# Kernel optimization log

Measured on AMD Instinct MI355X. Metric: run time of the kernel, lower is better.

The kernel has to match this reference:

```python
import jax, jax.numpy as jnp
from jax import lax
import numpy as np

B, T, D_IN, H, OUT = 64, 512, 512, 1024, 128


def setup_inputs() -> dict:
    key = jax.random.key(0)
    ks = jax.random.split(key, 12)
    s = 0.02
    return {
        "x": jax.random.normal(ks[0], (B, T, D_IN), dtype=jnp.float32),
        "W_ih0": jax.random.normal(ks[1], (H, D_IN), dtype=jnp.float32) * s,
        "W_hh0": jax.random.normal(ks[2], (H, H), dtype=jnp.float32) * s,
        "b_ih0": jax.random.normal(ks[3], (H,), dtype=jnp.float32) * s,
        "b_hh0": jax.random.normal(ks[4], (H,), dtype=jnp.float32) * s,
        "W_ih1": jax.random.normal(ks[5], (H, H), dtype=jnp.float32) * s,
        "W_hh1": jax.random.normal(ks[6], (H, H), dtype=jnp.float32) * s,
        "b_ih1": jax.random.normal(ks[7], (H,), dtype=jnp.float32) * s,
        "b_hh1": jax.random.normal(ks[8], (H,), dtype=jnp.float32) * s,
        "W_fc": jax.random.normal(ks[9], (OUT, H), dtype=jnp.float32) * s,
        "b_fc": jax.random.normal(ks[10], (OUT,), dtype=jnp.float32) * s,
    }


def _rnn_layer(seq, W_ih, W_hh, b_ih, b_hh):
    # seq: [B, T, D] -> outputs [B, T, H]; h_t = tanh(x_t W_ih^T + b_ih + h_{t-1} W_hh^T + b_hh)
    pre = jnp.einsum("btd,hd->bth", seq, W_ih) + b_ih + b_hh  # one big input GEMM
    h0 = jnp.zeros((seq.shape[0], W_hh.shape[0]), dtype=seq.dtype)

    def step(h, p_t):
        h_new = jnp.tanh(p_t + h @ W_hh.T)
        return h_new, h_new

    _, hs = lax.scan(step, h0, jnp.swapaxes(pre, 0, 1))  # [T, B, H]
    return jnp.swapaxes(hs, 0, 1)  # [B, T, H]


def reference(x, W_ih0, W_hh0, b_ih0, b_hh0, W_ih1, W_hh1, b_ih1, b_hh1, W_fc, b_fc):
    h1 = _rnn_layer(x, W_ih0, W_hh0, b_ih0, b_hh0)
    h2 = _rnn_layer(h1, W_ih1, W_hh1, b_ih1, b_hh1)
    last = h2[:, -1, :]  # [B, H]
    return last @ W_fc.T + b_fc  # [B, OUT]
```

## Files before the change

kernel.cpp:

```cpp
#include <hip/hip_runtime.h>
#include <stdint.h>
#include <stddef.h>

#define Bn   64
#define Tn   512
#define DINn 512
#define Hn   1024
#define OUTn 128

typedef __attribute__((ext_vector_type(4))) float f32x4;
typedef __attribute__((ext_vector_type(8))) short short8;
typedef __attribute__((ext_vector_type(4))) unsigned int u32x4;

__device__ __forceinline__ unsigned short f2bf(float f){
  unsigned int x = __builtin_bit_cast(unsigned int, f);
  x += 0x7fffu + ((x >> 16) & 1u);
  return (unsigned short)(x >> 16);
}
__device__ __forceinline__ float bf2f(unsigned short u){
  return __builtin_bit_cast(float, (unsigned int)u << 16);
}
__device__ __forceinline__ float tanh_fast(float v){
  float e = __expf(2.0f * v);
  return 1.0f - 2.0f / (e + 1.0f);
}

template<bool FAST>
__device__ __forceinline__ void st16(unsigned short* p, u32x4 v){
  if constexpr (FAST)
    asm volatile("global_store_dwordx4 %0, %1, off sc0" :: "v"(p), "v"(v) : "memory");
  else
    asm volatile("global_store_dwordx4 %0, %1, off sc0 sc1" :: "v"(p), "v"(v) : "memory");
}
__device__ __forceinline__ unsigned atom_poll(unsigned int* p){
  unsigned old, zero = 0;
  asm volatile("global_atomic_add %0, %1, %2, off sc0\n\t"
               "s_waitcnt vmcnt(0)"
               : "=&v"(old) : "v"(p), "v"(zero) : "memory");
  return old;
}
__device__ __forceinline__ void atom_poll2(unsigned int* p1, unsigned int* p2,
                                           unsigned &v1, unsigned &v2){
  unsigned zero = 0;
  asm volatile("global_atomic_add %0, %2, %4, off sc0\n\t"
               "global_atomic_add %1, %3, %4, off sc0\n\t"
               "s_waitcnt vmcnt(0)"
               : "=&v"(v1), "=&v"(v2)
               : "v"(p1), "v"(p2), "v"(zero) : "memory");
}
__device__ __forceinline__ void atom_inc(unsigned int* p){
  unsigned one = 1;
  asm volatile("global_atomic_add %0, %1, off" :: "v"(p), "v"(one) : "memory");
}
__device__ __forceinline__ unsigned ld1_sc0(const unsigned int* p){
  unsigned v;
  asm volatile("global_load_dword %0, %1, off sc0\n\t"
               "s_waitcnt vmcnt(0)" : "=&v"(v) : "v"(p) : "memory");
  return v;
}
__device__ __forceinline__ unsigned umin4(u32x4 a){
  unsigned m0 = a[0] < a[1] ? a[0] : a[1];
  unsigned m1 = a[2] < a[3] ? a[2] : a[3];
  return m0 < m1 ? m0 : m1;
}
__device__ __forceinline__ unsigned ld_line8_slow(const unsigned int* p){
  u32x4 a, b;
  asm volatile("global_load_dwordx4 %0, %2, off sc0 sc1\n\t"
               "global_load_dwordx4 %1, %3, off sc0 sc1\n\t"
               "s_waitcnt vmcnt(0)"
               : "=&v"(a), "=&v"(b) : "v"(p), "v"(p + 4) : "memory");
  unsigned ma = umin4(a), mb = umin4(b);
  return ma < mb ? ma : mb;
}
template<bool FAST>
__device__ __forceinline__ void wait_one(unsigned int* fc, unsigned int* fl, unsigned wf8, unsigned wslow){
  if constexpr (FAST){
    if (!wf8) return;
    for (int i = 0; i < (1 << 16); ++i){
      if (atom_poll(fc) >= wf8) return;
      __builtin_amdgcn_s_sleep(2);
    }
  } else {
    if (!wslow) return;
    for (int i = 0; i < (1 << 16); ++i){
      if (ld_line8_slow(fl) >= wslow) return;
      if (i > 16) __builtin_amdgcn_s_sleep(1);
    }
  }
}
template<bool FAST>
__device__ __forceinline__ void wait_dual(unsigned int* fc1, unsigned int* fl1, unsigned wf1, unsigned ws1,
                                          unsigned int* fc2, unsigned int* fl2, unsigned wf2, unsigned ws2){
  if constexpr (FAST){
    if (!wf2){ wait_one<true>(fc1, fl1, wf1, ws1); return; }
    for (int i = 0; i < (1 << 16); ++i){
      unsigned v1, v2;
      atom_poll2(fc1, fc2, v1, v2);
      if (v1 >= wf1 && v2 >= wf2) return;
      __builtin_amdgcn_s_sleep(2);
    }
  } else {
    if (!ws2){ wait_one<false>(fc1, fl1, wf1, ws1); return; }
    for (int i = 0; i < (1 << 16); ++i){
      if (ld_line8_slow(fl1) >= ws1 && ld_line8_slow(fl2) >= ws2) return;
      if (i > 16) __builtin_amdgcn_s_sleep(1);
    }
  }
}

template<bool FAST>
__device__ __forceinline__ void stage_lin(const unsigned short* base, unsigned short* hl, int tid){
  const unsigned short* p0 = base + (size_t)tid * 8;
  const unsigned short* p1 = p0 + 512 * 8;
  u32x4 v0, v1;
  if constexpr (FAST)
    asm volatile("global_load_dwordx4 %0, %2, off sc0\n\t"
                 "global_load_dwordx4 %1, %3, off sc0\n\t"
                 "s_waitcnt vmcnt(0)"
                 : "=&v"(v0), "=&v"(v1) : "v"(p0), "v"(p1) : "memory");
  else
    asm volatile("global_load_dwordx4 %0, %2, off sc0 sc1\n\t"
                 "global_load_dwordx4 %1, %3, off sc0 sc1\n\t"
                 "s_waitcnt vmcnt(0)"
                 : "=&v"(v0), "=&v"(v1) : "v"(p0), "v"(p1) : "memory");
  *(u32x4*)((char*)hl + tid * 16) = v0;
  *(u32x4*)((char*)hl + tid * 16 + 8192) = v1;
}
template<bool FAST>
__device__ __forceinline__ void ld4_chunk(const unsigned short* p, float* pv){
  unsigned u0,u1,u2,u3;
  if constexpr (FAST)
    asm volatile("global_load_ushort %0, %4, off sc0\n\t"
                 "global_load_ushort %1, %5, off sc0\n\t"
                 "global_load_ushort %2, %6, off sc0\n\t"
                 "global_load_ushort %3, %7, off sc0\n\t"
                 "s_waitcnt vmcnt(0)"
                 : "=&v"(u0), "=&v"(u1), "=&v"(u2), "=&v"(u3)
                 : "v"(p), "v"(p + 8), "v"(p + 16), "v"(p + 24) : "memory");
  else
    asm volatile("global_load_ushort %0, %4, off sc0 sc1\n\t"
                 "global_load_ushort %1, %5, off sc0 sc1\n\t"
                 "global_load_ushort %2, %6, off sc0 sc1\n\t"
                 "global_load_ushort %3, %7, off sc0 sc1\n\t"
                 "s_waitcnt vmcnt(0)"
                 : "=&v"(u0), "=&v"(u1), "=&v"(u2), "=&v"(u3)
                 : "v"(p), "v"(p + 8), "v"(p + 16), "v"(p + 24) : "memory");
  pv[0] = bf2f((unsigned short)u0); pv[1] = bf2f((unsigned short)u1);
  pv[2] = bf2f((unsigned short)u2); pv[3] = bf2f((unsigned short)u3);
}

__device__ __forceinline__ f32x4 mfma_tile(const char* lbase, const short8* wf, int lrow, int kh){
  f32x4 a0 = {0.f,0.f,0.f,0.f}, a1 = a0, a2 = a0, a3 = a0;
  int rb = kh * 128 + lrow * 16;
#pragma unroll
  for (int kk = 0; kk < 8; ++kk)
    a0 = __builtin_amdgcn_mfma_f32_16x16x32_bf16(*(const short8*)(lbase + kk*512 + rb), wf[kk], a0, 0,0,0);
#pragma unroll
  for (int kk = 8; kk < 16; ++kk)
    a1 = __builtin_amdgcn_mfma_f32_16x16x32_bf16(*(const short8*)(lbase + kk*512 + rb), wf[kk], a1, 0,0,0);
#pragma unroll
  for (int kk = 16; kk < 24; ++kk)
    a2 = __builtin_amdgcn_mfma_f32_16x16x32_bf16(*(const short8*)(lbase + kk*512 + rb), wf[kk], a2, 0,0,0);
#pragma unroll
  for (int kk = 24; kk < 32; ++kk)
    a3 = __builtin_amdgcn_mfma_f32_16x16x32_bf16(*(const short8*)(lbase + kk*512 + rb), wf[kk], a3, 0,0,0);
  return (a0 + a1) + (a2 + a3);
}

__global__ void cvt_bf16x8(const float* __restrict__ in, unsigned short* __restrict__ out,
                           long long n8){
  long long i = (long long)blockIdx.x * blockDim.x + threadIdx.x;
  long long stride = (long long)gridDim.x * blockDim.x;
  for (; i < n8; i += stride){
    const float* p = in + i*8;
    float4 a = *(const float4*)p;
    float4 b = *(const float4*)(p+4);
    short8 v;
    v[0]=(short)f2bf(a.x); v[1]=(short)f2bf(a.y); v[2]=(short)f2bf(a.z); v[3]=(short)f2bf(a.w);
    v[4]=(short)f2bf(b.x); v[5]=(short)f2bf(b.y); v[6]=(short)f2bf(b.z); v[7]=(short)f2bf(b.w);
    *(short8*)(out + i*8) = v;
  }
}

__global__ void bias_combine(const float* __restrict__ a, const float* __restrict__ b, float* __restrict__ o,
                             const float* __restrict__ c, const float* __restrict__ d, float* __restrict__ p){
  int i = blockIdx.x * blockDim.x + threadIdx.x;
  if (i < Hn){ o[i] = a[i] + b[i]; p[i] = c[i] + d[i]; }
}

__launch_bounds__(256, 2)
__global__ void gemm_pre0(const float* __restrict__ Av, const unsigned short* __restrict__ Bm,
                          const float* __restrict__ bias, unsigned short* __restrict__ C,
                          int N, int K)
{
  __shared__ unsigned short lA[128*64];
  __shared__ unsigned short lB[128*64];
  int bn = blockIdx.x, bm = blockIdx.y;
  int m0 = bm*128, n0 = bn*128;
  int tid = threadIdx.x, lane = tid & 63, w = tid >> 6;
  int wm = (w >> 1)*64, wn = (w & 1)*64;
  int cl = lane & 15, kh = lane >> 4;

  f32x4 acc[4][4];
  f32x4 z = {0.f,0.f,0.f,0.f};
#pragma unroll
  for (int i=0;i<4;i++)
#pragma unroll
    for (int j=0;j<4;j++) acc[i][j]=z;

  for (int k0 = 0; k0 < K; k0 += 64){
    __syncthreads();
#pragma unroll
    for (int r = 0; r < 4; ++r){
      int c = r*256 + tid;
      int row = c >> 3, cof = (c & 7)*8;
      const float* ap = Av + (size_t)(m0+row)*K + k0 + cof;
      float4 a = *(const float4*)ap;
      float4 b = *(const float4*)(ap+4);
      short8 v;
      v[0]=(short)f2bf(a.x); v[1]=(short)f2bf(a.y); v[2]=(short)f2bf(a.z); v[3]=(short)f2bf(a.w);
      v[4]=(short)f2bf(b.x); v[5]=(short)f2bf(b.y); v[6]=(short)f2bf(b.z); v[7]=(short)f2bf(b.w);
      *(short8*)&lA[row*64 + cof] = v;
      const unsigned short* bp = Bm + (size_t)(n0+row)*K + k0 + cof;
      *(short8*)&lB[row*64 + cof] = *(const short8*)bp;
    }
    __syncthreads();
#pragma unroll
    for (int kk = 0; kk < 2; ++kk){
      int kb = kk*32 + kh*8;
      short8 af[4], bfr[4];
#pragma unroll
      for (int i=0;i<4;i++) af[i]  = *(const short8*)&lA[(wm + i*16 + cl)*64 + kb];
#pragma unroll
      for (int j=0;j<4;j++) bfr[j] = *(const short8*)&lB[(wn + j*16 + cl)*64 + kb];
#pragma unroll
      for (int i=0;i<4;i++)
#pragma unroll
        for (int j=0;j<4;j++)
          acc[i][j] = __builtin_amdgcn_mfma_f32_16x16x32_bf16(af[i], bfr[j], acc[i][j], 0,0,0);
    }
  }
#pragma unroll
  for (int j=0;j<4;j++){
    int n = n0 + wn + j*16 + cl;
    float bs = bias[n];
#pragma unroll
    for (int i=0;i<4;i++){
      int mr = m0 + wm + i*16 + kh*4;
#pragma unroll
      for (int e=0;e<4;e++){
        int m = mr + e;
        int b = m >> 9, t = m & (Tn-1);
        C[((size_t)t*Bn + b)*N + n] = f2bf(acc[i][j][e] + bs);
      }
    }
  }
}

template<bool FAST>
__device__ __forceinline__ void rnn_body(
    int role, int g, int slot, int tid, int w, int lane, int cl, int kh, int lrow,
    const unsigned short* pre0, unsigned short* bufP, unsigned short* h1buf,
    const float* bias1,
    unsigned int* FCA0, unsigned int* FCA1, unsigned int* FCB, unsigned int* FCC,
    unsigned int* FLA, unsigned int* FLB, unsigned int* FLC,
    const short8* wf, unsigned short* hl, unsigned short* outl)
{
  const char* lbase = (const char*)hl;
  int n0 = slot*128 + w*16;
  int olocal = w*128 + ((cl>>3)*8 + kh*4)*8 + (cl&7);
  unsigned int* myFL = ((role == 0) ? FLA : (role == 1) ? FLB : FLC) + slot;

  for (int t = 0; t < Tn; ++t){
    float pv[4] = {0.f,0.f,0.f,0.f};
    if (role == 0 && kh < 2){
      const unsigned short* pp = pre0 + ((size_t)t*Bn + g*8 + kh*4)*Hn + n0 + cl;
#pragma unroll
      for (int j=0;j<4;j++) pv[j] = bf2f(pp[(size_t)j*Hn]);
    }
    if (tid == 0){
      if (role == 0)      wait_one <FAST>(FCA0, FLA, 8u*(unsigned)t, (unsigned)t);
      else if (role == 1) wait_one <FAST>(FCA1, FLA, 8u*(unsigned)(t+1), (unsigned)(t+1));
      else                wait_dual<FAST>(FCB, FLB, 8u*(unsigned)(t+1), (unsigned)(t+1),
                                          FCC, FLC, 8u*(unsigned)t, (unsigned)t);
    }
    __syncthreads();
    bool staged = true;
    if (role == 0){
      if (t > 0) stage_lin<FAST>(h1buf + ((size_t)(t+1)*8 + g)*8192, hl, tid);
      else staged = false;
    } else if (role == 1){
      stage_lin<FAST>(h1buf + ((size_t)(t+2)*8 + g)*8192, hl, tid);
    } else {
      if (kh < 2)
        ld4_chunk<FAST>(h1buf + ((size_t)t*8 + g)*8192 + slot*1024 + ((w*16+cl)>>3)*64 + kh*32 + (cl&7), pv);
      if (t > 0) stage_lin<FAST>(bufP + ((size_t)(t-1)*Bn + g*8)*Hn, hl, tid);
      else staged = false;
    }
    __syncthreads();
    f32x4 acc = {0.f,0.f,0.f,0.f};
    if (staged) acc = mfma_tile(lbase, wf, lrow, kh);
    if (kh < 2){
      float bs = (role == 1) ? bias1[n0 + cl] : 0.f;
#pragma unroll
      for (int j=0;j<4;j++){
        float v = acc[j] + pv[j] + bs;
        if (role != 1) v = tanh_fast(v);
        outl[olocal + j*8] = f2bf(v);
      }
    }
    unsigned short* tile;
    if (role == 0)      tile = h1buf + ((size_t)(t+2)*8 + g)*8192;
    else if (role == 1) tile = h1buf + ((size_t)t*8 + g)*8192;
    else                tile = bufP + ((size_t)t*Bn + g*8)*Hn;
    if (lane < 16){
      u32x4 v = *(const u32x4*)(outl + w*128 + lane*8);
      st16<FAST>(tile + slot*1024 + (w*16 + lane)*8, v);
    }
    asm volatile("s_waitcnt vmcnt(0)" ::: "memory");
    __syncthreads();
    if (tid == 0){
      if constexpr (FAST){
        if (role == 0){ atom_inc(FCA0); atom_inc(FCA1); }
        else if (role == 1) atom_inc(FCB);
        else atom_inc(FCC);
      } else {
        asm volatile("global_store_dword %0, %1, off sc0 sc1" :: "v"(myFL), "v"((unsigned)(t+1)) : "memory");
      }
    }
  }
}

__launch_bounds__(512, 2)
__global__ void rnn_fused(const unsigned short* __restrict__ pre0_ro,
                          unsigned short* __restrict__ bufP,
                          unsigned short* __restrict__ h1buf,
                          const float* __restrict__ Whh0,
                          const float* __restrict__ Wih1,
                          const float* __restrict__ Whh1,
                          const float* __restrict__ bias1,
                          unsigned int* ctrs)
{
  __shared__ __align__(16) unsigned short hl[8192];
  __shared__ __align__(16) unsigned short outl[1024];
  __shared__ int s_fast;
  int bx = blockIdx.x;
  int g = bx & 7;
  int sub = bx >> 3;
  int role = sub >> 3, slot = sub & 7;
  int tid = threadIdx.x, lane = tid & 63, w = tid >> 6;
  int n0 = slot*128 + w*16;
  int cl = lane & 15, kh = lane >> 4, lrow = cl & 7;
  unsigned int* FLA = ctrs + (0*8 + g)*32;
  unsigned int* FLB = ctrs + (1*8 + g)*32;
  unsigned int* FLC = ctrs + (2*8 + g)*32;
  unsigned int* arrive1 = ctrs + 768;
  unsigned int* badf    = ctrs + 772;
  unsigned int* arrive2 = ctrs + 776;
  unsigned int* FCA0 = ctrs + 1536 + (0*8 + g)*32;
  unsigned int* FCB  = ctrs + 1536 + (1*8 + g)*32;
  unsigned int* FCC  = ctrs + 1536 + (2*8 + g)*32;
  unsigned int* FCA1 = ctrs + 1536 + (3*8 + g)*32;

  if (tid == 0){
    int xcc;
    asm volatile("s_getreg_b32 %0, hwreg(HW_REG_XCC_ID)" : "=s"(xcc));
    unsigned int* testw = ctrs + 1024 + g*32;
    unsigned int* armed = testw + 16;
    if (xcc != g)
      __hip_atomic_fetch_or(badf, 1u, __ATOMIC_RELAXED, __HIP_MEMORY_SCOPE_AGENT);
    __hip_atomic_fetch_add(arrive1, 1u, __ATOMIC_ACQ_REL, __HIP_MEMORY_SCOPE_AGENT);
    int t1 = 0;
    for (int i = 0; i < (1 << 20); ++i){
      if (__hip_atomic_load(arrive1, __ATOMIC_ACQUIRE, __HIP_MEMORY_SCOPE_AGENT) >= 192u){ t1 = 1; break; }
      __builtin_amdgcn_s_sleep(2);
    }
    if (!t1) __hip_atomic_fetch_or(badf, 1u, __ATOMIC_RELAXED, __HIP_MEMORY_SCOPE_AGENT);
    unsigned magic = 0xC0FFEE00u | (unsigned)g;
    if (sub == 0){
      asm volatile("global_store_dword %0, %1, off sc0\n\t"
                   "s_waitcnt vmcnt(0)" :: "v"(testw), "v"(magic) : "memory");
      atom_inc(armed);
    }
    int ok = 0;
    for (int i = 0; i < (1 << 15); ++i){
      if (atom_poll(armed) >= 1u){ ok = (ld1_sc0(testw) == magic); break; }
      if (i > 16) __builtin_amdgcn_s_sleep(1);
    }
    if (!ok) __hip_atomic_fetch_or(badf, 1u, __ATOMIC_RELAXED, __HIP_MEMORY_SCOPE_AGENT);
    __hip_atomic_fetch_add(arrive2, 1u, __ATOMIC_ACQ_REL, __HIP_MEMORY_SCOPE_AGENT);
    int t2 = 0;
    for (int i = 0; i < (1 << 20); ++i){
      if (__hip_atomic_load(arrive2, __ATOMIC_ACQUIRE, __HIP_MEMORY_SCOPE_AGENT) >= 192u){ t2 = 1; break; }
      __builtin_amdgcn_s_sleep(2);
    }
    unsigned bad = __hip_atomic_load(badf, __ATOMIC_ACQUIRE, __HIP_MEMORY_SCOPE_AGENT);
    s_fast = (t2 && bad == 0u) ? 1 : 0;
  }
  __syncthreads();
  const bool fast = (s_fast != 0);

  const float* Wmat = (role == 0) ? Whh0 : (role == 1) ? Wih1 : Whh1;
  short8 wf[32];
  {
    const float* wr = Wmat + (size_t)(n0 + cl)*Hn + kh*8;
#pragma unroll
    for (int kk = 0; kk < 32; ++kk){
      float4 a = *(const float4*)(wr + kk*32);
      float4 b = *(const float4*)(wr + kk*32 + 4);
      short8 v;
      v[0]=(short)f2bf(a.x); v[1]=(short)f2bf(a.y); v[2]=(short)f2bf(a.z); v[3]=(short)f2bf(a.w);
      v[4]=(short)f2bf(b.x); v[5]=(short)f2bf(b.y); v[6]=(short)f2bf(b.z); v[7]=(short)f2bf(b.w);
      wf[kk] = v;
    }
  }

  if (fast)
    rnn_body<true >(role, g, slot, tid, w, lane, cl, kh, lrow, pre0_ro, bufP, h1buf,
                    bias1, FCA0, FCA1, FCB, FCC, FLA, FLB, FLC, wf, hl, outl);
  else
    rnn_body<false>(role, g, slot, tid, w, lane, cl, kh, lrow, pre0_ro, bufP, h1buf,
                    bias1, FCA0, FCA1, FCB, FCC, FLA, FLB, FLC, wf, hl, outl);
}

__global__ void fc_k(const unsigned short* __restrict__ bufP,
                     const float* __restrict__ Wfc, const float* __restrict__ bfc,
                     float* __restrict__ out)
{
  int gw = (blockIdx.x * blockDim.x + threadIdx.x) >> 6;
  int lane = threadIdx.x & 63;
  int b = gw >> 7, o = gw & 127;
  const unsigned short* tile = bufP + ((size_t)(Tn-1)*Bn + (b & ~7))*Hn;
  int r = b & 7;
  const float* wr = Wfc + (size_t)o*Hn;
  float s = 0.f;
  for (int k = lane; k < Hn; k += 64)
    s += bf2f(tile[((k>>3)*8 + r)*8 + (k&7)]) * wr[k];
#pragma unroll
  for (int off = 32; off > 0; off >>= 1) s += __shfl_down(s, off, 64);
  if (lane == 0) out[b*OUTn + o] = s + bfc[o];
}

extern "C" void kernel_launch(void* const* d_in, const int* in_sizes, int n_in,
                              void* d_out, int out_size, void* d_ws, size_t ws_size,
                              hipStream_t stream)
{
  const float* x    = (const float*)d_in[0];
  const float* Wih0 = (const float*)d_in[1];
  const float* Whh0 = (const float*)d_in[2];
  const float* bih0 = (const float*)d_in[3];
  const float* bhh0 = (const float*)d_in[4];
  const float* Wih1 = (const float*)d_in[5];
  const float* Whh1 = (const float*)d_in[6];
  const float* bih1 = (const float*)d_in[7];
  const float* bhh1 = (const float*)d_in[8];
  const float* Wfc  = (const float*)d_in[9];
  const float* bfc  = (const float*)d_in[10];
  float* out = (float*)d_out;

  unsigned short* bufP  = (unsigned short*)d_ws;
  unsigned short* h1buf = bufP  + (size_t)Bn*Tn*Hn;
  unsigned short* wih0b = h1buf + (size_t)(Tn+2)*8*8192;
  float* bias0 = (float*)(wih0b + (size_t)Hn*DINn);
  float* bias1 = bias0 + Hn;
  unsigned int* ctrs = (unsigned int*)(bias1 + Hn);

  hipMemsetAsync(ctrs, 0, 4096*sizeof(unsigned int), stream);

  cvt_bf16x8<<<256, 256, 0, stream>>>(Wih0, wih0b, (long long)Hn*DINn/8);
  bias_combine<<<4, 256, 0, stream>>>(bih0, bhh0, bias0, bih1, bhh1, bias1);

  dim3 g1(Hn/128, (Bn*Tn)/128);
  gemm_pre0<<<g1, 256, 0, stream>>>(x, wih0b, bias0, bufP, Hn, DINn);

  rnn_fused<<<192, 512, 0, stream>>>(bufP, bufP, h1buf, Whh0, Wih1, Whh1, bias1, ctrs);

  fc_k<<<2048, 256, 0, stream>>>(bufP, Wfc, bfc, out);
}
```

Measured before the change: 1.384 ms.

## Merge layer-1 input projection into layer-0 blocks and drop the third role

The layer-1 input-GEMM role is folded into the layer-0 workgroups. Each layer-0 block now holds both W_hh0 and W_ih1 fragments in registers and computes the projection of the previous h1 right after publishing the current h1 step. This cuts the grid from 192 to 128 blocks and removes one handoff hop. It also switches to per-wave arrival counters (64 per step), which drops the block-wide barrier before signaling. Layer-1 now fetches its h1 projection and staged tile in a single combined load batch, and the spin-wait sleeps less aggressively. The cost is doubled register pressure from the second weight set (launch bounds drop to 1 block per SM) and more serial work per layer-0 step on the critical recurrence path.

```diff
diff --git a/kernel.cpp b/kernel.cpp
--- a/kernel.cpp
+++ b/kernel.cpp
@@ -73,12 +73,12 @@
   return ma < mb ? ma : mb;
 }
 template<bool FAST>
-__device__ __forceinline__ void wait_one(unsigned int* fc, unsigned int* fl, unsigned wf8, unsigned wslow){
+__device__ __forceinline__ void wait_one(unsigned int* fc, unsigned int* fl, unsigned wfast, unsigned wslow){
   if constexpr (FAST){
-    if (!wf8) return;
+    if (!wfast) return;
     for (int i = 0; i < (1 << 16); ++i){
-      if (atom_poll(fc) >= wf8) return;
-      __builtin_amdgcn_s_sleep(2);
+      if (atom_poll(fc) >= wfast) return;
+      if (i > 8) __builtin_amdgcn_s_sleep(1);
     }
   } else {
     if (!wslow) return;
@@ -97,7 +97,7 @@
       unsigned v1, v2;
       atom_poll2(fc1, fc2, v1, v2);
       if (v1 >= wf1 && v2 >= wf2) return;
-      __builtin_amdgcn_s_sleep(2);
+      if (i > 8) __builtin_amdgcn_s_sleep(1);
     }
   } else {
     if (!ws2){ wait_one<false>(fc1, fl1, wf1, ws1); return; }
@@ -111,7 +111,7 @@
 template<bool FAST>
 __device__ __forceinline__ void stage_lin(const unsigned short* base, unsigned short* hl, int tid){
   const unsigned short* p0 = base + (size_t)tid * 8;
-  const unsigned short* p1 = p0 + 512 * 8;
+  const unsigned short* p1 = p0 + 4096;
   u32x4 v0, v1;
   if constexpr (FAST)
     asm volatile("global_load_dwordx4 %0, %2, off sc0\n\t"
@@ -125,6 +125,39 @@
                  : "=&v"(v0), "=&v"(v1) : "v"(p0), "v"(p1) : "memory");
   *(u32x4*)((char*)hl + tid * 16) = v0;
   *(u32x4*)((char*)hl + tid * 16 + 8192) = v1;
+}
+template<bool FAST>
+__device__ __forceinline__ void stage_ld4(const unsigned short* base, unsigned short* hl, int tid,
+                                          const unsigned short* p4, float* pv){
+  const unsigned short* p0 = base + (size_t)tid * 8;
+  const unsigned short* p1 = p0 + 4096;
+  u32x4 v0, v1; unsigned u0,u1,u2,u3;
+  if constexpr (FAST)
+    asm volatile(
+      "global_load_dwordx4 %0, %6, off sc0\n\t"
+      "global_load_dwordx4 %1, %7, off sc0\n\t"
+      "global_load_ushort %2, %8, off sc0\n\t"
+      "global_load_ushort %3, %9, off sc0\n\t"
+      "global_load_ushort %4, %10, off sc0\n\t"
+      "global_load_ushort %5, %11, off sc0\n\t"
+      "s_waitcnt vmcnt(0)"
+      : "=&v"(v0),"=&v"(v1),"=&v"(u0),"=&v"(u1),"=&v"(u2),"=&v"(u3)
+      : "v"(p0),"v"(p1),"v"(p4),"v"(p4+8),"v"(p4+16),"v"(p4+24) : "memory");
+  else
+    asm volatile(
+      "global_load_dwordx4 %0, %6, off sc0 sc1\n\t"
+      "global_load_dwordx4 %1, %7, off sc0 sc1\n\t"
+      "global_load_ushort %2, %8, off sc0 sc1\n\t"
+      "global_load_ushort %3, %9, off sc0 sc1\n\t"
+      "global_load_ushort %4, %10, off sc0 sc1\n\t"
+      "global_load_ushort %5, %11, off sc0 sc1\n\t"
+      "s_waitcnt vmcnt(0)"
+      : "=&v"(v0),"=&v"(v1),"=&v"(u0),"=&v"(u1),"=&v"(u2),"=&v"(u3)
+      : "v"(p0),"v"(p1),"v"(p4),"v"(p4+8),"v"(p4+16),"v"(p4+24) : "memory");
+  *(u32x4*)((char*)hl + tid * 16) = v0;
+  *(u32x4*)((char*)hl + tid * 16 + 8192) = v1;
+  pv[0] = bf2f((unsigned short)u0); pv[1] = bf2f((unsigned short)u1);
+  pv[2] = bf2f((unsigned short)u2); pv[3] = bf2f((unsigned short)u3);
 }
 template<bool FAST>
 __device__ __forceinline__ void ld4_chunk(const unsigned short* p, float* pv){
@@ -262,76 +295,119 @@
     int role, int g, int slot, int tid, int w, int lane, int cl, int kh, int lrow,
     const unsigned short* pre0, unsigned short* bufP, unsigned short* h1buf,
     const float* bias1,
-    unsigned int* FCA0, unsigned int* FCA1, unsigned int* FCB, unsigned int* FCC,
+    unsigned int* FCA, unsigned int* FCB, unsigned int* FCC,
     unsigned int* FLA, unsigned int* FLB, unsigned int* FLC,
-    const short8* wf, unsigned short* hl, unsigned short* outl)
+    const short8* wf, const short8* wf2, unsigned short* hl, unsigned short* outl)
 {
   const char* lbase = (const char*)hl;
   int n0 = slot*128 + w*16;
   int olocal = w*128 + ((cl>>3)*8 + kh*4)*8 + (cl&7);
-  unsigned int* myFL = ((role == 0) ? FLA : (role == 1) ? FLB : FLC) + slot;
-
-  for (int t = 0; t < Tn; ++t){
-    float pv[4] = {0.f,0.f,0.f,0.f};
-    if (role == 0 && kh < 2){
-      const unsigned short* pp = pre0 + ((size_t)t*Bn + g*8 + kh*4)*Hn + n0 + cl;
-#pragma unroll
-      for (int j=0;j<4;j++) pv[j] = bf2f(pp[(size_t)j*Hn]);
-    }
-    if (tid == 0){
-      if (role == 0)      wait_one <FAST>(FCA0, FLA, 8u*(unsigned)t, (unsigned)t);
-      else if (role == 1) wait_one <FAST>(FCA1, FLA, 8u*(unsigned)(t+1), (unsigned)(t+1));
-      else                wait_dual<FAST>(FCB, FLB, 8u*(unsigned)(t+1), (unsigned)(t+1),
-                                          FCC, FLC, 8u*(unsigned)t, (unsigned)t);
-    }
+  int khc = kh & 1;
+  int p4off = slot*1024 + ((w*16+cl)>>3)*64 + khc*32 + (cl&7);
+
+  if (role == 0){
+    float bs1 = bias1[n0 + cl];
+    for (int t = 0; t < Tn; ++t){
+      float pv[4] = {0.f,0.f,0.f,0.f};
+      if (kh < 2){
+        const unsigned short* pp = pre0 + ((size_t)t*Bn + g*8 + kh*4)*Hn + n0 + cl;
+#pragma unroll
+        for (int j=0;j<4;j++) pv[j] = bf2f(pp[(size_t)j*Hn]);
+      }
+      if (tid == 0) wait_one<FAST>(FCA, FLA, 64u*(unsigned)t, (unsigned)t);
+      __syncthreads();
+      if (t > 0) stage_lin<FAST>(h1buf + ((size_t)(t+1)*8 + g)*8192, hl, tid);
+      __syncthreads();
+      f32x4 acc = {0.f,0.f,0.f,0.f};
+      if (t > 0) acc = mfma_tile(lbase, wf, lrow, kh);
+      if (kh < 2){
+#pragma unroll
+        for (int j=0;j<4;j++) outl[olocal + j*8] = f2bf(tanh_fast(acc[j] + pv[j]));
+      }
+      unsigned short* tile = h1buf + ((size_t)(t+2)*8 + g)*8192;
+      if (lane < 16)
+        st16<FAST>(tile + slot*1024 + (w*16 + lane)*8, *(const u32x4*)(outl + w*128 + lane*8));
+      asm volatile("s_waitcnt vmcnt(0)" ::: "memory");
+      if constexpr (FAST){
+        if (lane == 0) atom_inc(FCA);
+      } else {
+        __syncthreads();
+        if (tid == 0)
+          asm volatile("global_store_dword %0, %1, off sc0 sc1" :: "v"(FLA+slot), "v"((unsigned)(t+1)) : "memory");
+      }
+      if (t > 0){
+        f32x4 acc2 = mfma_tile(lbase, wf2, lrow, kh);
+        if (kh < 2){
+#pragma unroll
+          for (int j=0;j<4;j++) outl[olocal + j*8] = f2bf(acc2[j] + bs1);
+        }
+        unsigned short* ptile = h1buf + ((size_t)(t-1)*8 + g)*8192;
+        if (lane < 16)
+          st16<FAST>(ptile + slot*1024 + (w*16 + lane)*8, *(const u32x4*)(outl + w*128 + lane*8));
+        asm volatile("s_waitcnt vmcnt(0)" ::: "memory");
+        if constexpr (FAST){
+          if (lane == 0) atom_inc(FCB);
+        } else {
+          __syncthreads();
+          if (tid == 0)
+            asm volatile("global_store_dword %0, %1, off sc0 sc1" :: "v"(FLB+slot), "v"((unsigned)t) : "memory");
+        }
+      }
+    }
+    if (tid == 0) wait_one<FAST>(FCA, FLA, 64u*(unsigned)Tn, (unsigned)Tn);
     __syncthreads();
-    bool staged = true;
-    if (role == 0){
-      if (t > 0) stage_lin<FAST>(h1buf + ((size_t)(t+1)*8 + g)*8192, hl, tid);
-      else staged = false;
-    } else if (role == 1){
-      stage_lin<FAST>(h1buf + ((size_t)(t+2)*8 + g)*8192, hl, tid);
+    stage_lin<FAST>(h1buf + ((size_t)(Tn+1)*8 + g)*8192, hl, tid);
+    __syncthreads();
+    f32x4 acc2 = mfma_tile(lbase, wf2, lrow, kh);
+    if (kh < 2){
+#pragma unroll
+      for (int j=0;j<4;j++) outl[olocal + j*8] = f2bf(acc2[j] + bs1);
+    }
+    unsigned short* ptile = h1buf + ((size_t)(Tn-1)*8 + g)*8192;
+    if (lane < 16)
+      st16<FAST>(ptile + slot*1024 + (w*16 + lane)*8, *(const u32x4*)(outl + w*128 + lane*8));
+    asm volatile("s_waitcnt vmcnt(0)" ::: "memory");
+    if constexpr (FAST){
+      if (lane == 0) atom_inc(FCB);
     } else {
-      if (kh < 2)
-        ld4_chunk<FAST>(h1buf + ((size_t)t*8 + g)*8192 + slot*1024 + ((w*16+cl)>>3)*64 + kh*32 + (cl&7), pv);
-      if (t > 0) stage_lin<FAST>(bufP + ((size_t)(t-1)*Bn + g*8)*Hn, hl, tid);
-      else staged = false;
-    }
-    __syncthreads();
-    f32x4 acc = {0.f,0.f,0.f,0.f};
-    if (staged) acc = mfma_tile(lbase, wf, lrow, kh);
-    if (kh < 2){
-      float bs = (role == 1) ? bias1[n0 + cl] : 0.f;
-#pragma unroll
-      for (int j=0;j<4;j++){
-        float v = acc[j] + pv[j] + bs;
-        if (role != 1) v = tanh_fast(v);
-        outl[olocal + j*8] = f2bf(v);
-      }
-    }
-    unsigned short* tile;
-    if (role == 0)      tile = h1buf + ((size_t)(t+2)*8 + g)*8192;
-    else if (role == 1) tile = h1buf + ((size_t)t*8 + g)*8192;
-    else                tile = bufP + ((size_t)t*Bn + g*8)*Hn;
-    if (lane < 16){
-      u32x4 v = *(const u32x4*)(outl + w*128 + lane*8);
-      st16<FAST>(tile + slot*1024 + (w*16 + lane)*8, v);
-    }
-    asm volatile("s_waitcnt vmcnt(0)" ::: "memory");
-    __syncthreads();
-    if (tid == 0){
+      __syncthreads();
+      if (tid == 0)
+        asm volatile("global_store_dword %0, %1, off sc0 sc1" :: "v"(FLB+slot), "v"((unsigned)Tn) : "memory");
+    }
+  } else {
+    for (int t = 0; t < Tn; ++t){
+      if (tid == 0) wait_dual<FAST>(FCB, FLB, 64u*(unsigned)(t+1), (unsigned)(t+1),
+                                    FCC, FLC, 64u*(unsigned)t, (unsigned)t);
+      __syncthreads();
+      float pv[4] = {0.f,0.f,0.f,0.f};
+      const unsigned short* p4 = h1buf + ((size_t)t*8 + g)*8192 + p4off;
+      if (t > 0)
+        stage_ld4<FAST>(bufP + ((size_t)(t-1)*Bn + g*8)*Hn, hl, tid, p4, pv);
+      else
+        ld4_chunk<FAST>(p4, pv);
+      __syncthreads();
+      f32x4 acc = {0.f,0.f,0.f,0.f};
+      if (t > 0) acc = mfma_tile(lbase, wf, lrow, kh);
+      if (kh < 2){
+#pragma unroll
+        for (int j=0;j<4;j++) outl[olocal + j*8] = f2bf(tanh_fast(acc[j] + pv[j]));
+      }
+      unsigned short* tile = bufP + ((size_t)t*Bn + g*8)*Hn;
+      if (lane < 16)
+        st16<FAST>(tile + slot*1024 + (w*16 + lane)*8, *(const u32x4*)(outl + w*128 + lane*8));
+      asm volatile("s_waitcnt vmcnt(0)" ::: "memory");
       if constexpr (FAST){
-        if (role == 0){ atom_inc(FCA0); atom_inc(FCA1); }
-        else if (role == 1) atom_inc(FCB);
-        else atom_inc(FCC);
+        if (lane == 0) atom_inc(FCC);
       } else {
-        asm volatile("global_store_dword %0, %1, off sc0 sc1" :: "v"(myFL), "v"((unsigned)(t+1)) : "memory");
-      }
-    }
-  }
-}
-
-__launch_bounds__(512, 2)
+        __syncthreads();
+        if (tid == 0)
+          asm volatile("global_store_dword %0, %1, off sc0 sc1" :: "v"(FLC+slot), "v"((unsigned)(t+1)) : "memory");
+      }
+    }
+  }
+}
+
+__launch_bounds__(512, 1)
 __global__ void rnn_fused(const unsigned short* __restrict__ pre0_ro,
                           unsigned short* __restrict__ bufP,
                           unsigned short* __restrict__ h1buf,
@@ -357,10 +433,9 @@
   unsigned int* arrive1 = ctrs + 768;
   unsigned int* badf    = ctrs + 772;
   unsigned int* arrive2 = ctrs + 776;
-  unsigned int* FCA0 = ctrs + 1536 + (0*8 + g)*32;
-  unsigned int* FCB  = ctrs + 1536 + (1*8 + g)*32;
-  unsigned int* FCC  = ctrs + 1536 + (2*8 + g)*32;
-  unsigned int* FCA1 = ctrs + 1536 + (3*8 + g)*32;
+  unsigned int* FCA = ctrs + 1536 + (0*8 + g)*32;
+  unsigned int* FCB = ctrs + 1536 + (1*8 + g)*32;
+  unsigned int* FCC = ctrs + 1536 + (2*8 + g)*32;
 
   if (tid == 0){
     int xcc;
@@ -372,7 +447,7 @@
     __hip_atomic_fetch_add(arrive1, 1u, __ATOMIC_ACQ_REL, __HIP_MEMORY_SCOPE_AGENT);
     int t1 = 0;
     for (int i = 0; i < (1 << 20); ++i){
-      if (__hip_atomic_load(arrive1, __ATOMIC_ACQUIRE, __HIP_MEMORY_SCOPE_AGENT) >= 192u){ t1 = 1; break; }
+      if (__hip_atomic_load(arrive1, __ATOMIC_ACQUIRE, __HIP_MEMORY_SCOPE_AGENT) >= 128u){ t1 = 1; break; }
       __builtin_amdgcn_s_sleep(2);
     }
     if (!t1) __hip_atomic_fetch_or(badf, 1u, __ATOMIC_RELAXED, __HIP_MEMORY_SCOPE_AGENT);
@@ -391,7 +466,7 @@
     __hip_atomic_fetch_add(arrive2, 1u, __ATOMIC_ACQ_REL, __HIP_MEMORY_SCOPE_AGENT);
     int t2 = 0;
     for (int i = 0; i < (1 << 20); ++i){
-      if (__hip_atomic_load(arrive2, __ATOMIC_ACQUIRE, __HIP_MEMORY_SCOPE_AGENT) >= 192u){ t2 = 1; break; }
+      if (__hip_atomic_load(arrive2, __ATOMIC_ACQUIRE, __HIP_MEMORY_SCOPE_AGENT) >= 128u){ t2 = 1; break; }
       __builtin_amdgcn_s_sleep(2);
     }
     unsigned bad = __hip_atomic_load(badf, __ATOMIC_ACQUIRE, __HIP_MEMORY_SCOPE_AGENT);
@@ -400,8 +475,8 @@
   __syncthreads();
   const bool fast = (s_fast != 0);
 
-  const float* Wmat = (role == 0) ? Whh0 : (role == 1) ? Wih1 : Whh1;
-  short8 wf[32];
+  const float* Wmat = (role == 0) ? Whh0 : Whh1;
+  short8 wf[32], wf2[32];
   {
     const float* wr = Wmat + (size_t)(n0 + cl)*Hn + kh*8;
 #pragma unroll
@@ -414,13 +489,25 @@
       wf[kk] = v;
     }
   }
+  if (role == 0){
+    const float* wr = Wih1 + (size_t)(n0 + cl)*Hn + kh*8;
+#pragma unroll
+    for (int kk = 0; kk < 32; ++kk){
+      float4 a = *(const float4*)(wr + kk*32);
+      float4 b = *(const float4*)(wr + kk*32 + 4);
+      short8 v;
+      v[0]=(short)f2bf(a.x); v[1]=(short)f2bf(a.y); v[2]=(short)f2bf(a.z); v[3]=(short)f2bf(a.w);
+      v[4]=(short)f2bf(b.x); v[5]=(short)f2bf(b.y); v[6]=(short)f2bf(b.z); v[7]=(short)f2bf(b.w);
+      wf2[kk] = v;
+    }
+  }
 
   if (fast)
     rnn_body<true >(role, g, slot, tid, w, lane, cl, kh, lrow, pre0_ro, bufP, h1buf,
-                    bias1, FCA0, FCA1, FCB, FCC, FLA, FLB, FLC, wf, hl, outl);
+                    bias1, FCA, FCB, FCC, FLA, FLB, FLC, wf, wf2, hl, outl);
   else
     rnn_body<false>(role, g, slot, tid, w, lane, cl, kh, lrow, pre0_ro, bufP, h1buf,
-                    bias1, FCA0, FCA1, FCB, FCC, FLA, FLB, FLC, wf, hl, outl);
+                    bias1, FCA, FCB, FCC, FLA, FLB, FLC, wf, wf2, hl, outl);
 }
 
 __global__ void fc_k(const unsigned short* __restrict__ bufP,
@@ -473,7 +560,7 @@
   dim3 g1(Hn/128, (Bn*Tn)/128);
   gemm_pre0<<<g1, 256, 0, stream>>>(x, wih0b, bias0, bufP, Hn, DINn);
 
-  rnn_fused<<<192, 512, 0, stream>>>(bufP, bufP, h1buf, Whh0, Wih1, Whh1, bias1, ctrs);
+  rnn_fused<<<128, 512, 0, stream>>>(bufP, bufP, h1buf, Whh0, Wih1, Whh1, bias1, ctrs);
 
   fc_k<<<2048, 256, 0, stream>>>(bufP, Wfc, bfc, out);
 }
```

After: 3.580 ms. +158.7%, slower.

## Split K across waves with LDS reduction and read h tiles directly from global

Applied to the files above, without the earlier changes.

Restructures the persistent RNN step so each wave computes two 16-column output tiles over half of K. MFMA A-operands are read straight from the global h buffer instead of being staged into LDS. A small LDS reduction then combines the two K halves, and only the first four waves apply bias and tanh and store. The change removes the LDS staging copy and one barrier-bound global-to-LDS pass per step. The trade is a partial-sum reduction, non-coherent-qualified direct global loads for the operands, and polling that spins with shorter sleeps.

```diff
diff --git a/kernel.cpp b/kernel.cpp
--- a/kernel.cpp
+++ b/kernel.cpp
@@ -23,6 +23,13 @@
 __device__ __forceinline__ float tanh_fast(float v){
   float e = __expf(2.0f * v);
   return 1.0f - 2.0f / (e + 1.0f);
+}
+__device__ __forceinline__ short8 packw(const float* p){
+  float4 a = *(const float4*)p; float4 b = *(const float4*)(p + 4);
+  short8 v;
+  v[0]=(short)f2bf(a.x); v[1]=(short)f2bf(a.y); v[2]=(short)f2bf(a.z); v[3]=(short)f2bf(a.w);
+  v[4]=(short)f2bf(b.x); v[5]=(short)f2bf(b.y); v[6]=(short)f2bf(b.z); v[7]=(short)f2bf(b.w);
+  return v;
 }
 
 template<bool FAST>
@@ -73,12 +80,12 @@
   return ma < mb ? ma : mb;
 }
 template<bool FAST>
-__device__ __forceinline__ void wait_one(unsigned int* fc, unsigned int* fl, unsigned wf8, unsigned wslow){
+__device__ __forceinline__ void wait_one(unsigned int* fc, unsigned int* fl, unsigned wfast, unsigned wslow){
   if constexpr (FAST){
-    if (!wf8) return;
+    if (!wfast) return;
     for (int i = 0; i < (1 << 16); ++i){
-      if (atom_poll(fc) >= wf8) return;
-      __builtin_amdgcn_s_sleep(2);
+      if (atom_poll(fc) >= wfast) return;
+      if (i > 8) __builtin_amdgcn_s_sleep(1);
     }
   } else {
     if (!wslow) return;
@@ -97,7 +104,7 @@
       unsigned v1, v2;
       atom_poll2(fc1, fc2, v1, v2);
       if (v1 >= wf1 && v2 >= wf2) return;
-      __builtin_amdgcn_s_sleep(2);
+      if (i > 8) __builtin_amdgcn_s_sleep(1);
     }
   } else {
     if (!ws2){ wait_one<false>(fc1, fl1, wf1, ws1); return; }
@@ -106,65 +113,6 @@
       if (i > 16) __builtin_amdgcn_s_sleep(1);
     }
   }
-}
-
-template<bool FAST>
-__device__ __forceinline__ void stage_lin(const unsigned short* base, unsigned short* hl, int tid){
-  const unsigned short* p0 = base + (size_t)tid * 8;
-  const unsigned short* p1 = p0 + 512 * 8;
-  u32x4 v0, v1;
-  if constexpr (FAST)
-    asm volatile("global_load_dwordx4 %0, %2, off sc0\n\t"
-                 "global_load_dwordx4 %1, %3, off sc0\n\t"
-                 "s_waitcnt vmcnt(0)"
-                 : "=&v"(v0), "=&v"(v1) : "v"(p0), "v"(p1) : "memory");
-  else
-    asm volatile("global_load_dwordx4 %0, %2, off sc0 sc1\n\t"
-                 "global_load_dwordx4 %1, %3, off sc0 sc1\n\t"
-                 "s_waitcnt vmcnt(0)"
-                 : "=&v"(v0), "=&v"(v1) : "v"(p0), "v"(p1) : "memory");
-  *(u32x4*)((char*)hl + tid * 16) = v0;
-  *(u32x4*)((char*)hl + tid * 16 + 8192) = v1;
-}
-template<bool FAST>
-__device__ __forceinline__ void ld4_chunk(const unsigned short* p, float* pv){
-  unsigned u0,u1,u2,u3;
-  if constexpr (FAST)
-    asm volatile("global_load_ushort %0, %4, off sc0\n\t"
-                 "global_load_ushort %1, %5, off sc0\n\t"
-                 "global_load_ushort %2, %6, off sc0\n\t"
-                 "global_load_ushort %3, %7, off sc0\n\t"
-                 "s_waitcnt vmcnt(0)"
-                 : "=&v"(u0), "=&v"(u1), "=&v"(u2), "=&v"(u3)
-                 : "v"(p), "v"(p + 8), "v"(p + 16), "v"(p + 24) : "memory");
-  else
-    asm volatile("global_load_ushort %0, %4, off sc0 sc1\n\t"
-                 "global_load_ushort %1, %5, off sc0 sc1\n\t"
-                 "global_load_ushort %2, %6, off sc0 sc1\n\t"
-                 "global_load_ushort %3, %7, off sc0 sc1\n\t"
-                 "s_waitcnt vmcnt(0)"
-                 : "=&v"(u0), "=&v"(u1), "=&v"(u2), "=&v"(u3)
-                 : "v"(p), "v"(p + 8), "v"(p + 16), "v"(p + 24) : "memory");
-  pv[0] = bf2f((unsigned short)u0); pv[1] = bf2f((unsigned short)u1);
-  pv[2] = bf2f((unsigned short)u2); pv[3] = bf2f((unsigned short)u3);
-}
-
-__device__ __forceinline__ f32x4 mfma_tile(const char* lbase, const short8* wf, int lrow, int kh){
-  f32x4 a0 = {0.f,0.f,0.f,0.f}, a1 = a0, a2 = a0, a3 = a0;
-  int rb = kh * 128 + lrow * 16;
-#pragma unroll
-  for (int kk = 0; kk < 8; ++kk)
-    a0 = __builtin_amdgcn_mfma_f32_16x16x32_bf16(*(const short8*)(lbase + kk*512 + rb), wf[kk], a0, 0,0,0);
-#pragma unroll
-  for (int kk = 8; kk < 16; ++kk)
-    a1 = __builtin_amdgcn_mfma_f32_16x16x32_bf16(*(const short8*)(lbase + kk*512 + rb), wf[kk], a1, 0,0,0);
-#pragma unroll
-  for (int kk = 16; kk < 24; ++kk)
-    a2 = __builtin_amdgcn_mfma_f32_16x16x32_bf16(*(const short8*)(lbase + kk*512 + rb), wf[kk], a2, 0,0,0);
-#pragma unroll
-  for (int kk = 24; kk < 32; ++kk)
-    a3 = __builtin_amdgcn_mfma_f32_16x16x32_bf16(*(const short8*)(lbase + kk*512 + rb), wf[kk], a3, 0,0,0);
-  return (a0 + a1) + (a2 + a3);
 }
 
 __global__ void cvt_bf16x8(const float* __restrict__ in, unsigned short* __restrict__ out,
@@ -264,19 +212,25 @@
     const float* bias1,
     unsigned int* FCA0, unsigned int* FCA1, unsigned int* FCB, unsigned int* FCC,
     unsigned int* FLA, unsigned int* FLB, unsigned int* FLC,
-    const short8* wf, unsigned short* hl, unsigned short* outl)
+    const short8* wfA, const short8* wfB,
+    unsigned short* outl, f32x4 (*red)[32])
 {
-  const char* lbase = (const char*)hl;
-  int n0 = slot*128 + w*16;
-  int olocal = w*128 + ((cl>>3)*8 + kh*4)*8 + (cl&7);
+  int t0 = 2*(w & 3);
+  int kb = (w >> 2) * 16;
+  int oA = t0*128 + ((cl>>3)*8 + kh*4)*8 + (cl&7);
   unsigned int* myFL = ((role == 0) ? FLA : (role == 1) ? FLB : FLC) + slot;
+  float bsA = 0.f, bsB = 0.f;
+  if (role == 1){
+    bsA = bias1[slot*128 + t0*16 + cl];
+    bsB = bias1[slot*128 + t0*16 + 16 + cl];
+  }
 
   for (int t = 0; t < Tn; ++t){
-    float pv[4] = {0.f,0.f,0.f,0.f};
-    if (role == 0 && kh < 2){
-      const unsigned short* pp = pre0 + ((size_t)t*Bn + g*8 + kh*4)*Hn + n0 + cl;
-#pragma unroll
-      for (int j=0;j<4;j++) pv[j] = bf2f(pp[(size_t)j*Hn]);
+    float pvA[4] = {0.f,0.f,0.f,0.f}, pvB[4] = {0.f,0.f,0.f,0.f};
+    if (role == 0 && w < 4 && kh < 2){
+      const unsigned short* pp = pre0 + ((size_t)t*Bn + g*8 + kh*4)*Hn + slot*128 + t0*16 + cl;
+#pragma unroll
+      for (int j=0;j<4;j++){ pvA[j] = bf2f(pp[(size_t)j*Hn]); pvB[j] = bf2f(pp[(size_t)j*Hn + 16]); }
     }
     if (tid == 0){
       if (role == 0)      wait_one <FAST>(FCA0, FLA, 8u*(unsigned)t, (unsigned)t);
@@ -285,37 +239,62 @@
                                           FCC, FLC, 8u*(unsigned)t, (unsigned)t);
     }
     __syncthreads();
-    bool staged = true;
-    if (role == 0){
-      if (t > 0) stage_lin<FAST>(h1buf + ((size_t)(t+1)*8 + g)*8192, hl, tid);
-      else staged = false;
-    } else if (role == 1){
-      stage_lin<FAST>(h1buf + ((size_t)(t+2)*8 + g)*8192, hl, tid);
-    } else {
-      if (kh < 2)
-        ld4_chunk<FAST>(h1buf + ((size_t)t*8 + g)*8192 + slot*1024 + ((w*16+cl)>>3)*64 + kh*32 + (cl&7), pv);
-      if (t > 0) stage_lin<FAST>(bufP + ((size_t)(t-1)*Bn + g*8)*Hn, hl, tid);
-      else staged = false;
+    asm volatile("" ::: "memory");
+
+    if (role == 2 && w < 4 && kh < 2){
+      const unsigned short* pb = h1buf + ((size_t)t*8 + g)*8192 + slot*1024;
+      const unsigned short* pA = pb + ((t0*16 + cl) >> 3)*64 + kh*32 + (cl & 7);
+      const unsigned short* pB = pb + (((t0+1)*16 + cl) >> 3)*64 + kh*32 + (cl & 7);
+#pragma unroll
+      for (int j=0;j<4;j++){ pvA[j] = bf2f(pA[j*8]); pvB[j] = bf2f(pB[j*8]); }
+    }
+
+    const unsigned short* fb = nullptr;
+    if (role == 0)      { if (t > 0) fb = h1buf + ((size_t)(t+1)*8 + g)*8192; }
+    else if (role == 1) fb = h1buf + ((size_t)(t+2)*8 + g)*8192;
+    else                { if (t > 0) fb = bufP + ((size_t)(t-1)*Bn + g*8)*Hn; }
+
+    f32x4 z = {0.f,0.f,0.f,0.f}, p0a = z, p0b = z, p1a = z, p1b = z;
+    if (fb){
+      const unsigned short* fp = fb + kb*256 + kh*64 + lrow*8;
+#pragma unroll
+      for (int q = 0; q < 16; q += 2){
+        short8 a0 = *(const short8*)(fp + q*256);
+        short8 a1 = *(const short8*)(fp + q*256 + 256);
+        p0a = __builtin_amdgcn_mfma_f32_16x16x32_bf16(a0, wfA[q],   p0a, 0,0,0);
+        p1a = __builtin_amdgcn_mfma_f32_16x16x32_bf16(a0, wfB[q],   p1a, 0,0,0);
+        p0b = __builtin_amdgcn_mfma_f32_16x16x32_bf16(a1, wfA[q+1], p0b, 0,0,0);
+        p1b = __builtin_amdgcn_mfma_f32_16x16x32_bf16(a1, wfB[q+1], p1b, 0,0,0);
+      }
+    }
+    f32x4 P0 = p0a + p0b, P1 = p1a + p1b;
+    if (w >= 4 && kh < 2){
+      red[(w-4)*2 + 0][kh*16 + cl] = P0;
+      red[(w-4)*2 + 1][kh*16 + cl] = P1;
     }
     __syncthreads();
-    f32x4 acc = {0.f,0.f,0.f,0.f};
-    if (staged) acc = mfma_tile(lbase, wf, lrow, kh);
-    if (kh < 2){
-      float bs = (role == 1) ? bias1[n0 + cl] : 0.f;
-#pragma unroll
-      for (int j=0;j<4;j++){
-        float v = acc[j] + pv[j] + bs;
-        if (role != 1) v = tanh_fast(v);
-        outl[olocal + j*8] = f2bf(v);
+    if (w < 4){
+      if (kh < 2){
+        P0 += red[w*2 + 0][kh*16 + cl];
+        P1 += red[w*2 + 1][kh*16 + cl];
+#pragma unroll
+        for (int j=0;j<4;j++){
+          float vA = P0[j] + pvA[j] + bsA;
+          float vB = P1[j] + pvB[j] + bsB;
+          if (role != 1){ vA = tanh_fast(vA); vB = tanh_fast(vB); }
+          outl[oA + j*8]       = f2bf(vA);
+          outl[oA + 128 + j*8] = f2bf(vB);
+        }
       }
-    }
-    unsigned short* tile;
-    if (role == 0)      tile = h1buf + ((size_t)(t+2)*8 + g)*8192;
-    else if (role == 1) tile = h1buf + ((size_t)t*8 + g)*8192;
-    else                tile = bufP + ((size_t)t*Bn + g*8)*Hn;
-    if (lane < 16){
-      u32x4 v = *(const u32x4*)(outl + w*128 + lane*8);
-      st16<FAST>(tile + slot*1024 + (w*16 + lane)*8, v);
+      unsigned short* tile;
+      if (role == 0)      tile = h1buf + ((size_t)(t+2)*8 + g)*8192;
+      else if (role == 1) tile = h1buf + ((size_t)t*8 + g)*8192;
+      else                tile = bufP + ((size_t)t*Bn + g*8)*Hn;
+      tile += slot*1024;
+      if (lane < 16){
+        st16<FAST>(tile + (t0*16 + lane)*8,     *(const u32x4*)(outl + t0*128 + lane*8));
+        st16<FAST>(tile + ((t0+1)*16 + lane)*8, *(const u32x4*)(outl + (t0+1)*128 + lane*8));
+      }
     }
     asm volatile("s_waitcnt vmcnt(0)" ::: "memory");
     __syncthreads();
@@ -341,15 +320,14 @@
                           const float* __restrict__ bias1,
                           unsigned int* ctrs)
 {
-  __shared__ __align__(16) unsigned short hl[8192];
   __shared__ __align__(16) unsigned short outl[1024];
+  __shared__ f32x4 red[8][32];
   __shared__ int s_fast;
   int bx = blockIdx.x;
   int g = bx & 7;
   int sub = bx >> 3;
   int role = sub >> 3, slot = sub & 7;
   int tid = threadIdx.x, lane = tid & 63, w = tid >> 6;
-  int n0 = slot*128 + w*16;
   int cl = lane & 15, kh = lane >> 4, lrow = cl & 7;
   unsigned int* FLA = ctrs + (0*8 + g)*32;
   unsigned int* FLB = ctrs + (1*8 + g)*32;
@@ -401,26 +379,25 @@
   const bool fast = (s_fast != 0);
 
   const float* Wmat = (role == 0) ? Whh0 : (role == 1) ? Wih1 : Whh1;
-  short8 wf[32];
+  int t0 = 2*(w & 3);
+  int kb = (w >> 2) * 16;
+  short8 wfA[16], wfB[16];
   {
-    const float* wr = Wmat + (size_t)(n0 + cl)*Hn + kh*8;
-#pragma unroll
-    for (int kk = 0; kk < 32; ++kk){
-      float4 a = *(const float4*)(wr + kk*32);
-      float4 b = *(const float4*)(wr + kk*32 + 4);
-      short8 v;
-      v[0]=(short)f2bf(a.x); v[1]=(short)f2bf(a.y); v[2]=(short)f2bf(a.z); v[3]=(short)f2bf(a.w);
-      v[4]=(short)f2bf(b.x); v[5]=(short)f2bf(b.y); v[6]=(short)f2bf(b.z); v[7]=(short)f2bf(b.w);
-      wf[kk] = v;
+    const float* wrA = Wmat + (size_t)(slot*128 + t0*16 + cl)*Hn + kb*32 + kh*8;
+    const float* wrB = wrA + (size_t)16*Hn;
+#pragma unroll
+    for (int q = 0; q < 16; ++q){
+      wfA[q] = packw(wrA + q*32);
+      wfB[q] = packw(wrB + q*32);
     }
   }
 
   if (fast)
     rnn_body<true >(role, g, slot, tid, w, lane, cl, kh, lrow, pre0_ro, bufP, h1buf,
-                    bias1, FCA0, FCA1, FCB, FCC, FLA, FLB, FLC, wf, hl, outl);
+                    bias1, FCA0, FCA1, FCB, FCC, FLA, FLB, FLC, wfA, wfB, outl, red);
   else
     rnn_body<false>(role, g, slot, tid, w, lane, cl, kh, lrow, pre0_ro, bufP, h1buf,
-                    bias1, FCA0, FCA1, FCB, FCC, FLA, FLB, FLC, wf, hl, outl);
+                    bias1, FCA0, FCA1, FCB, FCC, FLA, FLB, FLC, wfA, wfB, outl, red);
 }
 
 __global__ void fc_k(const unsigned short* __restrict__ bufP,
```

Result: slower. 1.807 ms (+30.6%).
